# Kernel optimization log

Measured on AMD Instinct MI355X. Metric: run time of the kernel, lower is better.

The kernel has to match this reference:

```python
import jax, jax.numpy as jnp
import numpy as np

B, OBS, L, D, BINS, HID = 4096, 128, 4, 8, 16, 512
S = L * D  # max_seq_len = 32; qchunk_size = S, single Q chunk


def _lin(k, i, o, s):
    kw, kb = jax.random.split(k)
    return jax.random.normal(kw, (i, o), jnp.float32) * s, jnp.zeros((o,), jnp.float32)


def setup_inputs() -> dict:
    key = jax.random.key(0)
    ks = jax.random.split(key, 12)
    inp = {
        "obs": jax.random.normal(ks[0], (B, OBS), jnp.float32),
        "category": jax.random.randint(ks[1], (B, L, D), 0, BINS, jnp.int32),
    }
    # v_network: obs_dim -> 512 -> 512 -> 512 -> 1 (tanh hidden)
    dims_v = [OBS, HID, HID, HID, 1]
    for i in range(4):
        w, b = _lin(ks[2 + i], dims_v[i], dims_v[i + 1], 0.05)
        inp[f"v_w{i}"], inp[f"v_b{i}"] = w, b
    # q_network: (obs_dim+actor_dim) -> 512 -> 512 -> 512 -> bins*S
    dims_q = [OBS + D, HID, HID, HID, BINS * S]
    for i in range(4):
        w, b = _lin(ks[6 + i], dims_q[i], dims_q[i + 1], 0.05)
        inp[f"q_w{i}"], inp[f"q_b{i}"] = w, b
    return inp


def _mlp(x, ws, bs):
    for w, b in zip(ws[:-1], bs[:-1]):
        x = jnp.tanh(x @ w + b)
    return x @ ws[-1] + bs[-1]


def _actions_from_category(category):
    # zoom_in per (level, dim): width_l = 2/bins^(l+1); low accumulates cat*width.
    cat = category.astype(jnp.float32)  # (B, L, D)
    widths = 2.0 / (jnp.float32(BINS) ** jnp.arange(1, L + 1, dtype=jnp.float32))  # (L,)
    cum_low = jnp.cumsum(cat * widths[None, :, None], axis=1)  # (B, L, D)
    mids = -1.0 + cum_low + 0.5 * widths[None, :, None]  # midpoint after each level
    # mids_full[:, j, d] = midpoint of dim d after j zoom-in updates (j=0 -> 0.0)
    mids_full = jnp.concatenate(
        [jnp.zeros((category.shape[0], 1, D), jnp.float32), mids], axis=1)  # (B, L+1, D)
    # at sequence step k (input to Q), dim d' has had U[k,d'] updates
    k = jnp.arange(S)
    U = k[:, None] // D + (jnp.arange(D)[None, :] < (k[:, None] % D)).astype(jnp.int32)  # (S, D)
    dgrid = jnp.broadcast_to(jnp.arange(D)[None, :], (S, D))
    return mids_full[:, U, dgrid]  # (B, S, D)


def reference(obs, category,
              v_w0, v_b0, v_w1, v_b1, v_w2, v_b2, v_w3, v_b3,
              q_w0, q_b0, q_w1, q_b1, q_w2, q_b2, q_w3, q_b3):
    vw = [v_w0, v_w1, v_w2, v_w3]; vb = [v_b0, v_b1, v_b2, v_b3]
    qw = [q_w0, q_w1, q_w2, q_w3]; qb = [q_b0, q_b1, q_b2, q_b3]
    b = obs.shape[0]
    actions = _actions_from_category(category)  # (B, S, D)
    obs_rep = jnp.broadcast_to(obs[:, None, :], (b, S, OBS))
    x = jnp.concatenate([obs_rep, actions], axis=-1)  # (B, S, OBS+D)
    adv = _mlp(x, qw, qb)  # (B, S, S*BINS)
    adv = adv.reshape(b, S, S, BINS)
    s_idx = jnp.arange(S)
    adv = adv[:, s_idx, s_idx, :]  # diagonal gather -> (B, S, BINS)
    adv = adv.reshape(b, L, D, BINS)
    value = _mlp(obs, vw, vb)  # (B, 1)
    nbias = jnp.zeros((b, L, D, 1), jnp.float32)  # use_nbias=False
    return value, adv, nbias
```

## Files before the change

kernel.cpp:

```cpp
#include <hip/hip_runtime.h>
#include <hip/hip_bf16.h>

#define B_SZ   4096
#define OBS_N  128
#define HID    512
#define TANH_SCALE 2.885390081777927f


typedef __bf16 bf16x8_t __attribute__((ext_vector_type(8)));
typedef float  f32x4_t  __attribute__((ext_vector_type(4)));

__device__ inline float fast_tanh(float x) {
    float e = __builtin_amdgcn_exp2f(x * TANH_SCALE);
    return fmaf(-2.f, __builtin_amdgcn_rcpf(e + 1.f), 1.f);
}

__device__ inline float fast_tanh_pre(float x) {
    float e = __builtin_amdgcn_exp2f(x);
    return fmaf(-2.f, __builtin_amdgcn_rcpf(e + 1.f), 1.f);
}

__device__ inline void gld_lds16(const void* g, void* l) {
    __builtin_amdgcn_global_load_lds(
        (const __attribute__((address_space(1))) void*)g,
        (__attribute__((address_space(3))) void*)l, 16, 0, 0);
}

__device__ inline int hs_off(int row, int col) {
    int c = col >> 3;
    int phys = (c & ~7) | ((c ^ (row & 7)) & 7);
    return row * 512 + phys * 8 + (col & 7);
}

__global__ __launch_bounds__(256) void prep_kernel(
    const float* __restrict__ obs, const int* __restrict__ category,
    const float* __restrict__ qw0, const float* __restrict__ qb0,
    const float* __restrict__ qw1, const float* __restrict__ qw2,
    const float* __restrict__ qw3,
    const float* __restrict__ vw0, const float* __restrict__ vb0,
    const float* __restrict__ vw1, const float* __restrict__ vw2,
    const float* __restrict__ qb1, const float* __restrict__ qb2,
    const float* __restrict__ vb1, const float* __restrict__ vb2,
    __hip_bfloat16* __restrict__ obs_bf,
    __hip_bfloat16* __restrict__ w0t, __hip_bfloat16* __restrict__ w1t,
    __hip_bfloat16* __restrict__ w2t, __hip_bfloat16* __restrict__ w3t,
    __hip_bfloat16* __restrict__ vw0t, __hip_bfloat16* __restrict__ vw1t,
    __hip_bfloat16* __restrict__ vw2t,
    __hip_bfloat16* __restrict__ w0aug, __hip_bfloat16* __restrict__ vw0aug,
    __hip_bfloat16* __restrict__ acts_bf, float* __restrict__ bias_s,
    float* __restrict__ nbias)
{
    const int bid = blockIdx.x, tid = threadIdx.x;
    if (bid < 512) {
        int i = bid * 1024 + tid * 4;
        float4 v = *(const float4*)&obs[i];
        union { __hip_bfloat16 b[4]; uint2 u; } o;
        o.b[0] = __float2bfloat16(v.x);
        o.b[1] = __float2bfloat16(v.y);
        o.b[2] = __float2bfloat16(v.z);
        o.b[3] = __float2bfloat16(v.w);
        *(uint2*)&obs_bf[i] = o.u;
    } else if (bid < 1024) {
        const float* src = (bid < 768) ? qw0 : vw0;
        __hip_bfloat16* dst = (bid < 768) ? w0t : vw0t;
        int idx = ((bid - 512) & 255) * 256 + tid;
        int n = idx >> 7, k = idx & 127;
        dst[idx] = __float2bfloat16(src[k * 512 + n] * TANH_SCALE);
    } else if (bid < 6144) {
        int job = (bid - 1024) >> 10;
        const float* srcs[5] = {qw1, qw2, qw3, vw1, vw2};
        __hip_bfloat16* dsts[5] = {w1t, w2t, w3t, vw1t, vw2t};
        float sc = (job == 2) ? 1.0f : TANH_SCALE;
        int idx = ((bid - 1024) & 1023) * 256 + tid;
        int e    = idx & 7;
        int lane = (idx >> 3) & 63;
        int tile, kc;
        if (job == 2) {
            kc   = (idx >> 9) & 15;
            tile = idx >> 13;
        } else {
            int jj = (idx >> 9) & 3;
            kc     = (idx >> 11) & 15;
            int g  = idx >> 15;
            tile = g * 4 + jj;
        }
        int k = kc * 32 + (lane >> 4) * 8 + e;
        int n = tile * 16 + (lane & 15);
        dsts[job][idx] = __float2bfloat16(srcs[job][k * 512 + n] * sc);
    } else if (bid < 10240) {
        int t = (bid - 6144) * 256 + tid;
        int d = t & 7;
        int r = t >> 3;
        int b = r & 4095, s = r >> 12;
        int U = (s >> 3) + ((d < (s & 7)) ? 1 : 0);
        float a = 0.f;
        if (U > 0) {
            float w = 0.125f, cum = 0.f;
            for (int j = 0; j < U; ++j) {
                cum += (float)category[b * 32 + j * 8 + d] * w;
                if (j == U - 1) a = -1.f + cum + 0.5f * w;
                w *= 0.0625f;
            }
        }
        acts_bf[t] = __float2bfloat16(a);
    } else if (bid < 10368) {
        int sub = bid - 10240;
        bool isv = sub >= 64;
        int idx = (sub & 63) * 256 + tid;
        int e    = idx & 7;
        int lane = (idx >> 3) & 63;
        int tile = idx >> 9;
        int k = (lane >> 4) * 8 + e;
        int n = tile * 16 + (lane & 15);
        float v = 0.f;
        if (!isv) {
            if (k < 8) v = qw0[(128 + k) * 512 + n];
            else if (k == 8) v = qb0[n];
            w0aug[idx] = __float2bfloat16(v * TANH_SCALE);
        } else {
            if (k == 8) v = vb0[n];
            vw0aug[idx] = __float2bfloat16(v * TANH_SCALE);
        }
    } else if (bid < 10376) {
        int idx = (bid - 10368) * 256 + tid;
        const float* srcs[4] = {qb1, qb2, vb1, vb2};
        bias_s[idx] = srcs[idx >> 9][idx & 511] * TANH_SCALE;
    } else {
        int i = (bid - 10376) * 1024 + tid * 4;
        float4 z = {0.f, 0.f, 0.f, 0.f};
        *(float4*)&nbias[i] = z;
    }
}

__global__ __launch_bounds__(256) void gemm_dual(
    const __hip_bfloat16* __restrict__ A0, const __hip_bfloat16* __restrict__ B0,
    const float* __restrict__ bias0, void* __restrict__ C0, int K0, int epi0, int nb0,
    const __hip_bfloat16* __restrict__ A1, const __hip_bfloat16* __restrict__ B1,
    const float* __restrict__ bias1, void* __restrict__ C1, int K1, int epi1)
{
    __shared__ __hip_bfloat16 As[128 * 32];
    __shared__ __hip_bfloat16 Bs[128 * 32];

    const __hip_bfloat16 *A, *Bt;
    const float* bias;
    void* Cout;
    int K, epi, tb;
    if ((int)blockIdx.x < nb0) {
        A = A0; Bt = B0; bias = bias0; Cout = C0; K = K0; epi = epi0; tb = blockIdx.x;
    } else {
        A = A1; Bt = B1; bias = bias1; Cout = C1; K = K1; epi = epi1; tb = blockIdx.x - nb0;
    }
    const long m0 = (long)(tb >> 2) * 128;
    const int  n0 = (tb & 3) * 128;

    const int tid  = threadIdx.x;
    const int wave = tid >> 6, lane = tid & 63;
    const int quad = lane >> 4, t = lane & 15;
    const int wr = wave >> 1, wc = wave & 1;

    f32x4_t acc[4][4] = {};

    const int lrow  = lane >> 2;
    const int lkoff = (((lane & 3) + (lane >> 3)) & 3) * 8;

    const __hip_bfloat16* Ag0 = A  + (m0 + wave * 32 +      lrow) * (long)K + lkoff;
    const __hip_bfloat16* Ag1 = A  + (m0 + wave * 32 + 16 + lrow) * (long)K + lkoff;
    const __hip_bfloat16* Bg0 = Bt + (long)(n0 + wave * 32 +      lrow) * K + lkoff;
    const __hip_bfloat16* Bg1 = Bt + (long)(n0 + wave * 32 + 16 + lrow) * K + lkoff;
    __hip_bfloat16* AsB0 = &As[(wave * 32) * 32];
    __hip_bfloat16* AsB1 = &As[(wave * 32 + 16) * 32];
    __hip_bfloat16* BsB0 = &Bs[(wave * 32) * 32];
    __hip_bfloat16* BsB1 = &Bs[(wave * 32 + 16) * 32];

    const int slot = ((quad - (t >> 1)) & 3) * 8;

    for (int k0 = 0; k0 < K; k0 += 32) {
        gld_lds16(Ag0 + k0, AsB0);
        gld_lds16(Ag1 + k0, AsB1);
        gld_lds16(Bg0 + k0, BsB0);
        gld_lds16(Bg1 + k0, BsB1);
        __syncthreads();
        bf16x8_t af[4], bfr[4];
        #pragma unroll
        for (int i = 0; i < 4; ++i)
            af[i] = *(const bf16x8_t*)&As[(wr * 64 + i * 16 + t) * 32 + slot];
        #pragma unroll
        for (int j = 0; j < 4; ++j)
            bfr[j] = *(const bf16x8_t*)&Bs[(wc * 64 + j * 16 + t) * 32 + slot];
        #pragma unroll
        for (int i = 0; i < 4; ++i)
            #pragma unroll
            for (int j = 0; j < 4; ++j)
                acc[i][j] = __builtin_amdgcn_mfma_f32_16x16x32_bf16(af[i], bfr[j], acc[i][j], 0, 0, 0);
        __syncthreads();
    }

    #pragma unroll
    for (int i = 0; i < 4; ++i) {
        const long rbase = m0 + wr * 64 + i * 16 + quad * 4;
        #pragma unroll
        for (int j = 0; j < 4; ++j) {
            const int col = n0 + wc * 64 + j * 16 + t;
            #pragma unroll
            for (int r = 0; r < 4; ++r) {
                float v = acc[i][j][r];
                if (epi == 1) {
                    v = fast_tanh(v + bias[col]);
                    ((__hip_bfloat16*)Cout)[(rbase + r) * 512 + col] = __float2bfloat16(v);
                } else if (epi == 2) {
                    ((__hip_bfloat16*)Cout)[(rbase + r) * 512 + col] = __float2bfloat16(v);
                } else if (epi == 3) {
                    const long m = rbase + r;
                    const int brow = (int)(m & 63);
                    const long idx =
                        ((((m >> 6) * 8 + (col >> 6)) * 16 + (brow >> 4) * 4 + ((col >> 4) & 3)) * 256)
                        + ((col >> 2) & 3) * 64 + (brow & 15) * 4 + (col & 3);
                    ((float*)Cout)[idx] = v;
                } else {
                    ((float*)Cout)[(rbase + r) * 512 + col] = v;
                }
            }
        }
    }
}

__device__ inline void epi_store(
    __hip_bfloat16* hs, f32x4_t acc[4][4],
    int n0w, int quad, int t)
{
    #pragma unroll
    for (int j = 0; j < 4; ++j) {
        const int oc0 = n0w + j * 16 + quad * 4;
        const int cbase = oc0 >> 3;
        const int sub = (quad & 1) * 4;
        #pragma unroll
        for (int rt = 0; rt < 4; ++rt) {
            const int row = rt * 16 + t;
            union { __hip_bfloat16 b[4]; uint2 v; } o;
            o.b[0] = __float2bfloat16(fast_tanh_pre(acc[rt][j][0]));
            o.b[1] = __float2bfloat16(fast_tanh_pre(acc[rt][j][1]));
            o.b[2] = __float2bfloat16(fast_tanh_pre(acc[rt][j][2]));
            o.b[3] = __float2bfloat16(fast_tanh_pre(acc[rt][j][3]));
            const int phys = (cbase & ~7) | ((cbase ^ (row & 7)) & 7);
            *(uint2*)&hs[row * 512 + phys * 8 + sub] = o.v;
        }
    }
}

__device__ inline void mfma_layer(
    __hip_bfloat16* hs, const __hip_bfloat16* __restrict__ Wt,
    const float* __restrict__ bias_s, int w, int lane)
{
    const int quad = lane >> 4, t = lane & 15;
    const int n0w = w * 64;
    const __hip_bfloat16* Wl = Wt + (size_t)w * 32768 + (size_t)lane * 8;
    f32x4_t acc[4][4];
    #pragma unroll
    for (int j = 0; j < 4; ++j) {
        const f32x4_t bv = *(const f32x4_t*)&bias_s[n0w + j * 16 + quad * 4];
        #pragma unroll
        for (int rt = 0; rt < 4; ++rt)
            acc[rt][j] = bv;
    }
    bf16x8_t wA[4], wB[4];
    #pragma unroll
    for (int j = 0; j < 4; ++j) {
        wA[j] = *(const bf16x8_t*)(Wl + (size_t)(0 * 4 + j) * 512);
        wB[j] = *(const bf16x8_t*)(Wl + (size_t)(1 * 4 + j) * 512);
    }

    for (int m = 0; m < 8; ++m) {
        {
            const int kc = 2 * m;
            const int craw = kc * 4 + quad;
            const int phys = (craw & ~7) | ((craw ^ (t & 7)) & 7);
            const __hip_bfloat16* hrow = &hs[t * 512 + phys * 8];
            bf16x8_t a0 = *(const bf16x8_t*)(hrow);
            bf16x8_t a1 = *(const bf16x8_t*)(hrow + 8192);
            __builtin_amdgcn_s_setprio(1);
            #pragma unroll
            for (int j = 0; j < 4; ++j) {
                acc[0][j] = __builtin_amdgcn_mfma_f32_16x16x32_bf16(wA[j], a0, acc[0][j], 0, 0, 0);
                acc[1][j] = __builtin_amdgcn_mfma_f32_16x16x32_bf16(wA[j], a1, acc[1][j], 0, 0, 0);
            }
            bf16x8_t a2 = *(const bf16x8_t*)(hrow + 2 * 8192);
            bf16x8_t a3 = *(const bf16x8_t*)(hrow + 3 * 8192);
            #pragma unroll
            for (int j = 0; j < 4; ++j) {
                acc[2][j] = __builtin_amdgcn_mfma_f32_16x16x32_bf16(wA[j], a2, acc[2][j], 0, 0, 0);
                acc[3][j] = __builtin_amdgcn_mfma_f32_16x16x32_bf16(wA[j], a3, acc[3][j], 0, 0, 0);
            }
            __builtin_amdgcn_s_setprio(0);
            if (m < 7) {
                #pragma unroll
                for (int j = 0; j < 4; ++j)
                    wA[j] = *(const bf16x8_t*)(Wl + (size_t)((kc + 2) * 4 + j) * 512);
            }
        }
        {
            const int kc = 2 * m + 1;
            const int craw = kc * 4 + quad;
            const int phys = (craw & ~7) | ((craw ^ (t & 7)) & 7);
            const __hip_bfloat16* hrow = &hs[t * 512 + phys * 8];
            bf16x8_t a0 = *(const bf16x8_t*)(hrow);
            bf16x8_t a1 = *(const bf16x8_t*)(hrow + 8192);
            __builtin_amdgcn_s_setprio(1);
            #pragma unroll
            for (int j = 0; j < 4; ++j) {
                acc[0][j] = __builtin_amdgcn_mfma_f32_16x16x32_bf16(wB[j], a0, acc[0][j], 0, 0, 0);
                acc[1][j] = __builtin_amdgcn_mfma_f32_16x16x32_bf16(wB[j], a1, acc[1][j], 0, 0, 0);
            }
            bf16x8_t a2 = *(const bf16x8_t*)(hrow + 2 * 8192);
            bf16x8_t a3 = *(const bf16x8_t*)(hrow + 3 * 8192);
            #pragma unroll
            for (int j = 0; j < 4; ++j) {
                acc[2][j] = __builtin_amdgcn_mfma_f32_16x16x32_bf16(wB[j], a2, acc[2][j], 0, 0, 0);
                acc[3][j] = __builtin_amdgcn_mfma_f32_16x16x32_bf16(wB[j], a3, acc[3][j], 0, 0, 0);
            }
            __builtin_amdgcn_s_setprio(0);
            if (m < 7) {
                #pragma unroll
                for (int j = 0; j < 4; ++j)
                    wB[j] = *(const bf16x8_t*)(Wl + (size_t)((kc + 2) * 4 + j) * 512);
            }
        }
    }
    __syncthreads();
    epi_store(hs, acc, n0w, quad, t);
    __syncthreads();
}

__global__ __launch_bounds__(512, 4) void fused_kernel(
    const float* __restrict__ p,
    const float* __restrict__ pv,
    const __hip_bfloat16* __restrict__ acts_bf,
    const __hip_bfloat16* __restrict__ w0aug,
    const __hip_bfloat16* __restrict__ vw0aug,
    const __hip_bfloat16* __restrict__ w1t, const float* __restrict__ qb1s,
    const __hip_bfloat16* __restrict__ w2t, const float* __restrict__ qb2s,
    const __hip_bfloat16* __restrict__ w3t, const float* __restrict__ qb3,
    float* __restrict__ advout,
    const __hip_bfloat16* __restrict__ vw1t, const float* __restrict__ vb1s,
    const __hip_bfloat16* __restrict__ vw2t, const float* __restrict__ vb2s,
    const float* __restrict__ vw3, const float* __restrict__ vb3,
    float* __restrict__ vout)
{
    __shared__ __hip_bfloat16 hs[64 * 512];
    const int bid = blockIdx.x;
    const int tid = threadIdx.x;
    const int w = tid >> 6, lane = tid & 63;
    const int quad = lane >> 4, t = lane & 15;
    const bool is_q = bid < 2048;
    const int s  = is_q ? (bid >> 6) : 0;
    const int mb = is_q ? (bid & 63) : (bid - 2048);
    const int n0w = w * 64;

    {
        const float* Pt = (is_q ? p : pv) + (((size_t)mb * 8 + w) * 16) * 256 + lane * 4;
        const __hip_bfloat16* W0 = is_q ? w0aug : vw0aug;
        f32x4_t acc[4][4];
        #pragma unroll
        for (int rt = 0; rt < 4; ++rt)
            #pragma unroll
            for (int j = 0; j < 4; ++j)
                acc[rt][j] = *(const f32x4_t*)(Pt + (rt * 4 + j) * 256);
        bf16x8_t bfrag[4];
        #pragma unroll
        for (int rt = 0; rt < 4; ++rt) {
            union { bf16x8_t vec; unsigned short u[8]; } bu;
            #pragma unroll
            for (int i = 0; i < 8; ++i) bu.u[i] = 0;
            if (quad == 1) bu.u[0] = 0x3F80;
            if (is_q && quad == 0) {
                const long r = (long)s * 4096 + mb * 64 + rt * 16 + t;
                bu.vec = *(const bf16x8_t*)&acts_bf[r * 8];
            }
            bfrag[rt] = bu.vec;
        }
        bf16x8_t wq[4];
        #pragma unroll
        for (int j = 0; j < 4; ++j)
            wq[j] = *(const bf16x8_t*)(W0 + ((size_t)(w * 4 + j) * 64 + lane) * 8);
        __builtin_amdgcn_s_setprio(1);
        #pragma unroll
        for (int j = 0; j < 4; ++j)
            #pragma unroll
            for (int rt = 0; rt < 4; ++rt)
                acc[rt][j] = __builtin_amdgcn_mfma_f32_16x16x32_bf16(wq[j], bfrag[rt], acc[rt][j], 0, 0, 0);
        __builtin_amdgcn_s_setprio(0);
        epi_store(hs, acc, n0w, quad, t);
    }
    __syncthreads();

    mfma_layer(hs, is_q ? w1t : vw1t, is_q ? qb1s : vb1s, w, lane);
    mfma_layer(hs, is_q ? w2t : vw2t, is_q ? qb2s : vb2s, w, lane);

    if (is_q) {
        f32x4_t acc = {};
        {
            const __hip_bfloat16* W3l = w3t + ((size_t)s * 16 * 64 + (size_t)lane) * 8;
            const int kc0 = (w >> 2) * 8;
            const int wrow = (w & 3) * 16 + t;
            #pragma unroll
            for (int kk = 0; kk < 8; ++kk) {
                const int kc = kc0 + kk;
                const int craw = kc * 4 + quad;
                const int phys = (craw & ~7) | ((craw ^ (t & 7)) & 7);
                bf16x8_t a = *(const bf16x8_t*)&hs[wrow * 512 + phys * 8];
                bf16x8_t bq = *(const bf16x8_t*)(W3l + (size_t)kc * 512);
                acc = __builtin_amdgcn_mfma_f32_16x16x32_bf16(a, bq, acc, 0, 0, 0);
            }
        }
        __syncthreads();
        float* hsf = (float*)hs;
        {
            const float add = (w < 4) ? qb3[s * 16 + t] : 0.f;
            const int base = (w >> 2) * 1024;
            #pragma unroll
            for (int rr = 0; rr < 4; ++rr)
                hsf[base + ((w & 3) * 16 + quad * 4 + rr) * 16 + t] = acc[rr] + add;
        }
        __syncthreads();
        const int row = tid >> 3, cp = tid & 7;
        float2 lo = *(const float2*)&hsf[row * 16 + cp * 2];
        float2 hi = *(const float2*)&hsf[1024 + row * 16 + cp * 2];
        float2 v2 = {lo.x + hi.x, lo.y + hi.y};
        *(float2*)&advout[(size_t)(mb * 64 + row) * 512 + s * 16 + cp * 2] = v2;
    } else {
        const int row = tid >> 3, seg = tid & 7;
        float sum = 0.f;
        for (int k = seg * 64; k < seg * 64 + 64; ++k)
            sum += __bfloat162float(hs[hs_off(row, k)]) * vw3[k];
        sum += __shfl_xor(sum, 1);
        sum += __shfl_xor(sum, 2);
        sum += __shfl_xor(sum, 4);
        if (seg == 0) vout[mb * 64 + row] = sum + vb3[0];
    }
}

extern "C" void kernel_launch(void* const* d_in, const int* in_sizes, int n_in,
                              void* d_out, int out_size, void* d_ws, size_t ws_size,
                              hipStream_t stream) {
    const float* obs      = (const float*)d_in[0];
    const int*   category = (const int*)d_in[1];
    const float* v_w0 = (const float*)d_in[2];
    const float* v_b0 = (const float*)d_in[3];
    const float* v_w1 = (const float*)d_in[4];
    const float* v_b1 = (const float*)d_in[5];
    const float* v_w2 = (const float*)d_in[6];
    const float* v_b2 = (const float*)d_in[7];
    const float* v_w3 = (const float*)d_in[8];
    const float* v_b3 = (const float*)d_in[9];
    const float* q_w0 = (const float*)d_in[10];
    const float* q_b0 = (const float*)d_in[11];
    const float* q_w1 = (const float*)d_in[12];
    const float* q_b1 = (const float*)d_in[13];
    const float* q_w2 = (const float*)d_in[14];
    const float* q_b2 = (const float*)d_in[15];
    const float* q_w3 = (const float*)d_in[16];
    const float* q_b3 = (const float*)d_in[17];

    char* ws = (char*)d_ws;
    __hip_bfloat16* obs_bf = (__hip_bfloat16*)(ws + 0);
    __hip_bfloat16* w0t    = (__hip_bfloat16*)(ws + 1048576);
    __hip_bfloat16* vw0t   = (__hip_bfloat16*)(ws + 1179648);
    __hip_bfloat16* w1t    = (__hip_bfloat16*)(ws + 1310720);
    __hip_bfloat16* w2t    = (__hip_bfloat16*)(ws + 1835008);
    __hip_bfloat16* w3t    = (__hip_bfloat16*)(ws + 2359296);
    __hip_bfloat16* vw1t   = (__hip_bfloat16*)(ws + 2883584);
    __hip_bfloat16* vw2t   = (__hip_bfloat16*)(ws + 3407872);
    __hip_bfloat16* w0aug  = (__hip_bfloat16*)(ws + 3932160);
    __hip_bfloat16* vw0aug = (__hip_bfloat16*)(ws + 3964928);
    __hip_bfloat16* acts_bf= (__hip_bfloat16*)(ws + 3997696);
    float*          p      = (float*)         (ws + 6094848);
    float*          pv     = (float*)         (ws + 14483456);
    float*          bias_s = (float*)         (ws + 22872064);

    float* out       = (float*)d_out;
    float* out_value = out;
    float* out_adv   = out + 4096;
    float* out_nbias = out + 4096 + (size_t)B_SZ * 512;

    prep_kernel<<<10504, 256, 0, stream>>>(
        obs, category, q_w0, q_b0, q_w1, q_w2, q_w3, v_w0, v_b0, v_w1, v_w2,
        q_b1, q_b2, v_b1, v_b2,
        obs_bf, w0t, w1t, w2t, w3t, vw0t, vw1t, vw2t, w0aug, vw0aug,
        acts_bf, bias_s, out_nbias);

    gemm_dual<<<256, 256, 0, stream>>>(
        obs_bf, w0t, nullptr, p, 128, 3, 128,
        obs_bf, vw0t, nullptr, pv, 128, 3);

    fused_kernel<<<2112, 512, 0, stream>>>(
        p, pv, acts_bf, w0aug, vw0aug,
        w1t, bias_s, w2t, bias_s + 512, w3t, q_b3, out_adv,
        vw1t, bias_s + 1024, vw2t, bias_s + 1536, v_w3, v_b3, out_value);
}
```

Measured before the change: 253.5 us.

## Fold first-layer obs GEMM into fused kernel, dropping separate gemm_dual pass

Removes the standalone gemm_dual launch that precomputed obs@W0 into fp32 workspace buffers, which the fused kernel then reloaded per sequence step. Instead each fused block computes the obs projection directly with MFMA over K=128, plus the action/bias augmentation chunk, using a new K-chunked pre-tiled W0 layout built in prep. This saves a kernel launch and about 16MB of fp32 intermediate write+read. In exchange it recomputes the obs projection for every sequence step (32x redundant MFMA work for the Q path).

```diff
diff --git a/kernel.cpp b/kernel.cpp
--- a/kernel.cpp
+++ b/kernel.cpp
@@ -10,20 +10,9 @@
 typedef __bf16 bf16x8_t __attribute__((ext_vector_type(8)));
 typedef float  f32x4_t  __attribute__((ext_vector_type(4)));
 
-__device__ inline float fast_tanh(float x) {
-    float e = __builtin_amdgcn_exp2f(x * TANH_SCALE);
-    return fmaf(-2.f, __builtin_amdgcn_rcpf(e + 1.f), 1.f);
-}
-
 __device__ inline float fast_tanh_pre(float x) {
     float e = __builtin_amdgcn_exp2f(x);
     return fmaf(-2.f, __builtin_amdgcn_rcpf(e + 1.f), 1.f);
-}
-
-__device__ inline void gld_lds16(const void* g, void* l) {
-    __builtin_amdgcn_global_load_lds(
-        (const __attribute__((address_space(1))) void*)g,
-        (__attribute__((address_space(3))) void*)l, 16, 0, 0);
 }
 
 __device__ inline int hs_off(int row, int col) {
@@ -42,11 +31,10 @@
     const float* __restrict__ qb1, const float* __restrict__ qb2,
     const float* __restrict__ vb1, const float* __restrict__ vb2,
     __hip_bfloat16* __restrict__ obs_bf,
-    __hip_bfloat16* __restrict__ w0t, __hip_bfloat16* __restrict__ w1t,
-    __hip_bfloat16* __restrict__ w2t, __hip_bfloat16* __restrict__ w3t,
-    __hip_bfloat16* __restrict__ vw0t, __hip_bfloat16* __restrict__ vw1t,
-    __hip_bfloat16* __restrict__ vw2t,
-    __hip_bfloat16* __restrict__ w0aug, __hip_bfloat16* __restrict__ vw0aug,
+    __hip_bfloat16* __restrict__ w1t, __hip_bfloat16* __restrict__ w2t,
+    __hip_bfloat16* __restrict__ w3t,
+    __hip_bfloat16* __restrict__ vw1t, __hip_bfloat16* __restrict__ vw2t,
+    __hip_bfloat16* __restrict__ w0ta, __hip_bfloat16* __restrict__ vw0ta,
     __hip_bfloat16* __restrict__ acts_bf, float* __restrict__ bias_s,
     float* __restrict__ nbias)
 {
@@ -60,18 +48,12 @@
         o.b[2] = __float2bfloat16(v.z);
         o.b[3] = __float2bfloat16(v.w);
         *(uint2*)&obs_bf[i] = o.u;
-    } else if (bid < 1024) {
-        const float* src = (bid < 768) ? qw0 : vw0;
-        __hip_bfloat16* dst = (bid < 768) ? w0t : vw0t;
-        int idx = ((bid - 512) & 255) * 256 + tid;
-        int n = idx >> 7, k = idx & 127;
-        dst[idx] = __float2bfloat16(src[k * 512 + n] * TANH_SCALE);
-    } else if (bid < 6144) {
-        int job = (bid - 1024) >> 10;
+    } else if (bid < 5632) {
+        int job = (bid - 512) >> 10;
         const float* srcs[5] = {qw1, qw2, qw3, vw1, vw2};
         __hip_bfloat16* dsts[5] = {w1t, w2t, w3t, vw1t, vw2t};
         float sc = (job == 2) ? 1.0f : TANH_SCALE;
-        int idx = ((bid - 1024) & 1023) * 256 + tid;
+        int idx = ((bid - 512) & 1023) * 256 + tid;
         int e    = idx & 7;
         int lane = (idx >> 3) & 63;
         int tile, kc;
@@ -87,8 +69,8 @@
         int k = kc * 32 + (lane >> 4) * 8 + e;
         int n = tile * 16 + (lane & 15);
         dsts[job][idx] = __float2bfloat16(srcs[job][k * 512 + n] * sc);
-    } else if (bid < 10240) {
-        int t = (bid - 6144) * 256 + tid;
+    } else if (bid < 9728) {
+        int t = (bid - 5632) * 256 + tid;
         int d = t & 7;
         int r = t >> 3;
         int b = r & 4095, s = r >> 12;
@@ -104,22 +86,24 @@
         }
         acts_bf[t] = __float2bfloat16(a);
     } else if (bid < 10368) {
-        int sub = bid - 10240;
-        bool isv = sub >= 64;
-        int idx = (sub & 63) * 256 + tid;
+        int sub = bid - 9728;
+        bool isv = sub >= 320;
+        int idx = (isv ? sub - 320 : sub) * 256 + tid;
         int e    = idx & 7;
         int lane = (idx >> 3) & 63;
-        int tile = idx >> 9;
-        int k = (lane >> 4) * 8 + e;
-        int n = tile * 16 + (lane & 15);
+        int j    = (idx >> 9) & 3;
+        int kcw  = idx >> 11;
+        int k = (kcw % 5) * 32 + (lane >> 4) * 8 + e;
+        int n = ((kcw / 5) * 4 + j) * 16 + (lane & 15);
         float v = 0.f;
         if (!isv) {
-            if (k < 8) v = qw0[(128 + k) * 512 + n];
-            else if (k == 8) v = qb0[n];
-            w0aug[idx] = __float2bfloat16(v * TANH_SCALE);
+            if (k < 136) v = qw0[k * 512 + n];
+            else if (k == 136) v = qb0[n];
+            w0ta[idx] = __float2bfloat16(v * TANH_SCALE);
         } else {
-            if (k == 8) v = vb0[n];
-            vw0aug[idx] = __float2bfloat16(v * TANH_SCALE);
+            if (k < 128) v = vw0[k * 512 + n];
+            else if (k == 136) v = vb0[n];
+            vw0ta[idx] = __float2bfloat16(v * TANH_SCALE);
         }
     } else if (bid < 10376) {
         int idx = (bid - 10368) * 256 + tid;
@@ -129,98 +113,6 @@
         int i = (bid - 10376) * 1024 + tid * 4;
         float4 z = {0.f, 0.f, 0.f, 0.f};
         *(float4*)&nbias[i] = z;
-    }
-}
-
-__global__ __launch_bounds__(256) void gemm_dual(
-    const __hip_bfloat16* __restrict__ A0, const __hip_bfloat16* __restrict__ B0,
-    const float* __restrict__ bias0, void* __restrict__ C0, int K0, int epi0, int nb0,
-    const __hip_bfloat16* __restrict__ A1, const __hip_bfloat16* __restrict__ B1,
-    const float* __restrict__ bias1, void* __restrict__ C1, int K1, int epi1)
-{
-    __shared__ __hip_bfloat16 As[128 * 32];
-    __shared__ __hip_bfloat16 Bs[128 * 32];
-
-    const __hip_bfloat16 *A, *Bt;
-    const float* bias;
-    void* Cout;
-    int K, epi, tb;
-    if ((int)blockIdx.x < nb0) {
-        A = A0; Bt = B0; bias = bias0; Cout = C0; K = K0; epi = epi0; tb = blockIdx.x;
-    } else {
-        A = A1; Bt = B1; bias = bias1; Cout = C1; K = K1; epi = epi1; tb = blockIdx.x - nb0;
-    }
-    const long m0 = (long)(tb >> 2) * 128;
-    const int  n0 = (tb & 3) * 128;
-
-    const int tid  = threadIdx.x;
-    const int wave = tid >> 6, lane = tid & 63;
-    const int quad = lane >> 4, t = lane & 15;
-    const int wr = wave >> 1, wc = wave & 1;
-
-    f32x4_t acc[4][4] = {};
-
-    const int lrow  = lane >> 2;
-    const int lkoff = (((lane & 3) + (lane >> 3)) & 3) * 8;
-
-    const __hip_bfloat16* Ag0 = A  + (m0 + wave * 32 +      lrow) * (long)K + lkoff;
-    const __hip_bfloat16* Ag1 = A  + (m0 + wave * 32 + 16 + lrow) * (long)K + lkoff;
-    const __hip_bfloat16* Bg0 = Bt + (long)(n0 + wave * 32 +      lrow) * K + lkoff;
-    const __hip_bfloat16* Bg1 = Bt + (long)(n0 + wave * 32 + 16 + lrow) * K + lkoff;
-    __hip_bfloat16* AsB0 = &As[(wave * 32) * 32];
-    __hip_bfloat16* AsB1 = &As[(wave * 32 + 16) * 32];
-    __hip_bfloat16* BsB0 = &Bs[(wave * 32) * 32];
-    __hip_bfloat16* BsB1 = &Bs[(wave * 32 + 16) * 32];
-
-    const int slot = ((quad - (t >> 1)) & 3) * 8;
-
-    for (int k0 = 0; k0 < K; k0 += 32) {
-        gld_lds16(Ag0 + k0, AsB0);
-        gld_lds16(Ag1 + k0, AsB1);
-        gld_lds16(Bg0 + k0, BsB0);
-        gld_lds16(Bg1 + k0, BsB1);
-        __syncthreads();
-        bf16x8_t af[4], bfr[4];
-        #pragma unroll
-        for (int i = 0; i < 4; ++i)
-            af[i] = *(const bf16x8_t*)&As[(wr * 64 + i * 16 + t) * 32 + slot];
-        #pragma unroll
-        for (int j = 0; j < 4; ++j)
-            bfr[j] = *(const bf16x8_t*)&Bs[(wc * 64 + j * 16 + t) * 32 + slot];
-        #pragma unroll
-        for (int i = 0; i < 4; ++i)
-            #pragma unroll
-            for (int j = 0; j < 4; ++j)
-                acc[i][j] = __builtin_amdgcn_mfma_f32_16x16x32_bf16(af[i], bfr[j], acc[i][j], 0, 0, 0);
-        __syncthreads();
-    }
-
-    #pragma unroll
-    for (int i = 0; i < 4; ++i) {
-        const long rbase = m0 + wr * 64 + i * 16 + quad * 4;
-        #pragma unroll
-        for (int j = 0; j < 4; ++j) {
-            const int col = n0 + wc * 64 + j * 16 + t;
-            #pragma unroll
-            for (int r = 0; r < 4; ++r) {
-                float v = acc[i][j][r];
-                if (epi == 1) {
-                    v = fast_tanh(v + bias[col]);
-                    ((__hip_bfloat16*)Cout)[(rbase + r) * 512 + col] = __float2bfloat16(v);
-                } else if (epi == 2) {
-                    ((__hip_bfloat16*)Cout)[(rbase + r) * 512 + col] = __float2bfloat16(v);
-                } else if (epi == 3) {
-                    const long m = rbase + r;
-                    const int brow = (int)(m & 63);
-                    const long idx =
-                        ((((m >> 6) * 8 + (col >> 6)) * 16 + (brow >> 4) * 4 + ((col >> 4) & 3)) * 256)
-                        + ((col >> 2) & 3) * 64 + (brow & 15) * 4 + (col & 3);
-                    ((float*)Cout)[idx] = v;
-                } else {
-                    ((float*)Cout)[(rbase + r) * 512 + col] = v;
-                }
-            }
-        }
     }
 }
 
@@ -331,11 +223,10 @@
 }
 
 __global__ __launch_bounds__(512, 4) void fused_kernel(
-    const float* __restrict__ p,
-    const float* __restrict__ pv,
+    const __hip_bfloat16* __restrict__ obs_bf,
     const __hip_bfloat16* __restrict__ acts_bf,
-    const __hip_bfloat16* __restrict__ w0aug,
-    const __hip_bfloat16* __restrict__ vw0aug,
+    const __hip_bfloat16* __restrict__ w0ta,
+    const __hip_bfloat16* __restrict__ vw0ta,
     const __hip_bfloat16* __restrict__ w1t, const float* __restrict__ qb1s,
     const __hip_bfloat16* __restrict__ w2t, const float* __restrict__ qb2s,
     const __hip_bfloat16* __restrict__ w3t, const float* __restrict__ qb3,
@@ -356,38 +247,81 @@
     const int n0w = w * 64;
 
     {
-        const float* Pt = (is_q ? p : pv) + (((size_t)mb * 8 + w) * 16) * 256 + lane * 4;
-        const __hip_bfloat16* W0 = is_q ? w0aug : vw0aug;
-        f32x4_t acc[4][4];
+        const __hip_bfloat16* W0 = is_q ? w0ta : vw0ta;
+        const __hip_bfloat16* Wl = W0 + (size_t)w * 10240 + (size_t)lane * 8;
+        const __hip_bfloat16* ob = obs_bf + ((size_t)(mb * 64) + t) * 128 + quad * 8;
+        f32x4_t acc[4][4] = {};
+        bf16x8_t wA[4], wB[4];
         #pragma unroll
-        for (int rt = 0; rt < 4; ++rt)
+        for (int j = 0; j < 4; ++j) {
+            wA[j] = *(const bf16x8_t*)(Wl + (size_t)(0 * 4 + j) * 512);
+            wB[j] = *(const bf16x8_t*)(Wl + (size_t)(1 * 4 + j) * 512);
+        }
+        #pragma unroll
+        for (int m = 0; m < 2; ++m) {
+            {
+                const int kc = 2 * m;
+                bf16x8_t a0 = *(const bf16x8_t*)(ob + 0 * 16 * 128 + kc * 32);
+                bf16x8_t a1 = *(const bf16x8_t*)(ob + 1 * 16 * 128 + kc * 32);
+                bf16x8_t a2 = *(const bf16x8_t*)(ob + 2 * 16 * 128 + kc * 32);
+                bf16x8_t a3 = *(const bf16x8_t*)(ob + 3 * 16 * 128 + kc * 32);
+                __builtin_amdgcn_s_setprio(1);
+                #pragma unroll
+                for (int j = 0; j < 4; ++j) {
+                    acc[0][j] = __builtin_amdgcn_mfma_f32_16x16x32_bf16(wA[j], a0, acc[0][j], 0, 0, 0);
+                    acc[1][j] = __builtin_amdgcn_mfma_f32_16x16x32_bf16(wA[j], a1, acc[1][j], 0, 0, 0);
+                    acc[2][j] = __builtin_amdgcn_mfma_f32_16x16x32_bf16(wA[j], a2, acc[2][j], 0, 0, 0);
+                    acc[3][j] = __builtin_amdgcn_mfma_f32_16x16x32_bf16(wA[j], a3, acc[3][j], 0, 0, 0);
+                }
+                __builtin_amdgcn_s_setprio(0);
+                #pragma unroll
+                for (int j = 0; j < 4; ++j)
+                    wA[j] = *(const bf16x8_t*)(Wl + (size_t)((kc + 2) * 4 + j) * 512);
+            }
+            {
+                const int kc = 2 * m + 1;
+                bf16x8_t a0 = *(const bf16x8_t*)(ob + 0 * 16 * 128 + kc * 32);
+                bf16x8_t a1 = *(const bf16x8_t*)(ob + 1 * 16 * 128 + kc * 32);
+                bf16x8_t a2 = *(const bf16x8_t*)(ob + 2 * 16 * 128 + kc * 32);
+                bf16x8_t a3 = *(const bf16x8_t*)(ob + 3 * 16 * 128 + kc * 32);
+                __builtin_amdgcn_s_setprio(1);
+                #pragma unroll
+                for (int j = 0; j < 4; ++j) {
+                    acc[0][j] = __builtin_amdgcn_mfma_f32_16x16x32_bf16(wB[j], a0, acc[0][j], 0, 0, 0);
+                    acc[1][j] = __builtin_amdgcn_mfma_f32_16x16x32_bf16(wB[j], a1, acc[1][j], 0, 0, 0);
+                    acc[2][j] = __builtin_amdgcn_mfma_f32_16x16x32_bf16(wB[j], a2, acc[2][j], 0, 0, 0);
+                    acc[3][j] = __builtin_amdgcn_mfma_f32_16x16x32_bf16(wB[j], a3, acc[3][j], 0, 0, 0);
+                }
+                __builtin_amdgcn_s_setprio(0);
+                if (m == 0) {
+                    #pragma unroll
+                    for (int j = 0; j < 4; ++j)
+                        wB[j] = *(const bf16x8_t*)(Wl + (size_t)(3 * 4 + j) * 512);
+                }
+            }
+        }
+        {
+            bf16x8_t bfrag[4];
+            #pragma unroll
+            for (int rt = 0; rt < 4; ++rt) {
+                union { bf16x8_t vec; unsigned short u[8]; } bu;
+                #pragma unroll
+                for (int i = 0; i < 8; ++i) bu.u[i] = 0;
+                if (quad == 1) bu.u[0] = 0x3F80;
+                if (is_q && quad == 0) {
+                    const long r = (long)s * 4096 + mb * 64 + rt * 16 + t;
+                    bu.vec = *(const bf16x8_t*)&acts_bf[r * 8];
+                }
+                bfrag[rt] = bu.vec;
+            }
+            __builtin_amdgcn_s_setprio(1);
             #pragma unroll
             for (int j = 0; j < 4; ++j)
-                acc[rt][j] = *(const f32x4_t*)(Pt + (rt * 4 + j) * 256);
-        bf16x8_t bfrag[4];
-        #pragma unroll
-        for (int rt = 0; rt < 4; ++rt) {
-            union { bf16x8_t vec; unsigned short u[8]; } bu;
-            #pragma unroll
-            for (int i = 0; i < 8; ++i) bu.u[i] = 0;
-            if (quad == 1) bu.u[0] = 0x3F80;
-            if (is_q && quad == 0) {
-                const long r = (long)s * 4096 + mb * 64 + rt * 16 + t;
-                bu.vec = *(const bf16x8_t*)&acts_bf[r * 8];
-            }
-            bfrag[rt] = bu.vec;
-        }
-        bf16x8_t wq[4];
-        #pragma unroll
-        for (int j = 0; j < 4; ++j)
-            wq[j] = *(const bf16x8_t*)(W0 + ((size_t)(w * 4 + j) * 64 + lane) * 8);
-        __builtin_amdgcn_s_setprio(1);
-        #pragma unroll
-        for (int j = 0; j < 4; ++j)
-            #pragma unroll
-            for (int rt = 0; rt < 4; ++rt)
-                acc[rt][j] = __builtin_amdgcn_mfma_f32_16x16x32_bf16(wq[j], bfrag[rt], acc[rt][j], 0, 0, 0);
-        __builtin_amdgcn_s_setprio(0);
+                #pragma unroll
+                for (int rt = 0; rt < 4; ++rt)
+                    acc[rt][j] = __builtin_amdgcn_mfma_f32_16x16x32_bf16(wA[j], bfrag[rt], acc[rt][j], 0, 0, 0);
+            __builtin_amdgcn_s_setprio(0);
+        }
         epi_store(hs, acc, n0w, quad, t);
     }
     __syncthreads();
@@ -462,19 +396,15 @@
 
     char* ws = (char*)d_ws;
     __hip_bfloat16* obs_bf = (__hip_bfloat16*)(ws + 0);
-    __hip_bfloat16* w0t    = (__hip_bfloat16*)(ws + 1048576);
-    __hip_bfloat16* vw0t   = (__hip_bfloat16*)(ws + 1179648);
-    __hip_bfloat16* w1t    = (__hip_bfloat16*)(ws + 1310720);
-    __hip_bfloat16* w2t    = (__hip_bfloat16*)(ws + 1835008);
-    __hip_bfloat16* w3t    = (__hip_bfloat16*)(ws + 2359296);
-    __hip_bfloat16* vw1t   = (__hip_bfloat16*)(ws + 2883584);
-    __hip_bfloat16* vw2t   = (__hip_bfloat16*)(ws + 3407872);
-    __hip_bfloat16* w0aug  = (__hip_bfloat16*)(ws + 3932160);
-    __hip_bfloat16* vw0aug = (__hip_bfloat16*)(ws + 3964928);
+    __hip_bfloat16* w1t    = (__hip_bfloat16*)(ws + 1048576);
+    __hip_bfloat16* w2t    = (__hip_bfloat16*)(ws + 1572864);
+    __hip_bfloat16* w3t    = (__hip_bfloat16*)(ws + 2097152);
+    __hip_bfloat16* vw1t   = (__hip_bfloat16*)(ws + 2621440);
+    __hip_bfloat16* vw2t   = (__hip_bfloat16*)(ws + 3145728);
+    __hip_bfloat16* w0ta   = (__hip_bfloat16*)(ws + 3670016);
+    __hip_bfloat16* vw0ta  = (__hip_bfloat16*)(ws + 3833856);
     __hip_bfloat16* acts_bf= (__hip_bfloat16*)(ws + 3997696);
-    float*          p      = (float*)         (ws + 6094848);
-    float*          pv     = (float*)         (ws + 14483456);
-    float*          bias_s = (float*)         (ws + 22872064);
+    float*          bias_s = (float*)         (ws + 6094848);
 
     float* out       = (float*)d_out;
     float* out_value = out;
@@ -484,15 +414,11 @@
     prep_kernel<<<10504, 256, 0, stream>>>(
         obs, category, q_w0, q_b0, q_w1, q_w2, q_w3, v_w0, v_b0, v_w1, v_w2,
         q_b1, q_b2, v_b1, v_b2,
-        obs_bf, w0t, w1t, w2t, w3t, vw0t, vw1t, vw2t, w0aug, vw0aug,
+        obs_bf, w1t, w2t, w3t, vw1t, vw2t, w0ta, vw0ta,
         acts_bf, bias_s, out_nbias);
 
-    gemm_dual<<<256, 256, 0, stream>>>(
-        obs_bf, w0t, nullptr, p, 128, 3, 128,
-        obs_bf, vw0t, nullptr, pv, 128, 3);
-
     fused_kernel<<<2112, 512, 0, stream>>>(
-        p, pv, acts_bf, w0aug, vw0aug,
+        obs_bf, acts_bf, w0ta, vw0ta,
         w1t, bias_s, w2t, bias_s + 512, w3t, q_b3, out_adv,
         vw1t, bias_s + 1024, vw2t, bias_s + 1536, v_w3, v_b3, out_value);
 }
```

After: 259.4 us. 2.3% more time.

## Fold first-layer obs GEMM into prep kernel with on-the-fly bf16 conversion

Applied to the files above, without the earlier changes.

Removes the separate gemm_dual launch and the obs/w0 bf16 staging buffers. The first 256 blocks of prep_kernel now compute the obs x W0 products directly, converting fp32 obs and scaled, transposed W0 to bf16 while filling LDS. This saves one kernel launch and a round trip through global memory for the converted operands. In exchange the loads are strided scalar fp32 reads with no async LDS copy, and the GEMM blocks share a launch with the prep blocks.

```diff
diff --git a/kernel.cpp b/kernel.cpp
--- a/kernel.cpp
+++ b/kernel.cpp
@@ -10,20 +10,9 @@
 typedef __bf16 bf16x8_t __attribute__((ext_vector_type(8)));
 typedef float  f32x4_t  __attribute__((ext_vector_type(4)));
 
-__device__ inline float fast_tanh(float x) {
-    float e = __builtin_amdgcn_exp2f(x * TANH_SCALE);
-    return fmaf(-2.f, __builtin_amdgcn_rcpf(e + 1.f), 1.f);
-}
-
 __device__ inline float fast_tanh_pre(float x) {
     float e = __builtin_amdgcn_exp2f(x);
     return fmaf(-2.f, __builtin_amdgcn_rcpf(e + 1.f), 1.f);
-}
-
-__device__ inline void gld_lds16(const void* g, void* l) {
-    __builtin_amdgcn_global_load_lds(
-        (const __attribute__((address_space(1))) void*)g,
-        (__attribute__((address_space(3))) void*)l, 16, 0, 0);
 }
 
 __device__ inline int hs_off(int row, int col) {
@@ -41,37 +30,112 @@
     const float* __restrict__ vw1, const float* __restrict__ vw2,
     const float* __restrict__ qb1, const float* __restrict__ qb2,
     const float* __restrict__ vb1, const float* __restrict__ vb2,
-    __hip_bfloat16* __restrict__ obs_bf,
-    __hip_bfloat16* __restrict__ w0t, __hip_bfloat16* __restrict__ w1t,
-    __hip_bfloat16* __restrict__ w2t, __hip_bfloat16* __restrict__ w3t,
-    __hip_bfloat16* __restrict__ vw0t, __hip_bfloat16* __restrict__ vw1t,
-    __hip_bfloat16* __restrict__ vw2t,
+    __hip_bfloat16* __restrict__ w1t, __hip_bfloat16* __restrict__ w2t,
+    __hip_bfloat16* __restrict__ w3t,
+    __hip_bfloat16* __restrict__ vw1t, __hip_bfloat16* __restrict__ vw2t,
     __hip_bfloat16* __restrict__ w0aug, __hip_bfloat16* __restrict__ vw0aug,
     __hip_bfloat16* __restrict__ acts_bf, float* __restrict__ bias_s,
-    float* __restrict__ nbias)
+    float* __restrict__ nbias,
+    float* __restrict__ p, float* __restrict__ pv)
 {
+    __shared__ __hip_bfloat16 Asg[128 * 32];
+    __shared__ __hip_bfloat16 Bsg[128 * 32];
     const int bid = blockIdx.x, tid = threadIdx.x;
-    if (bid < 512) {
-        int i = bid * 1024 + tid * 4;
-        float4 v = *(const float4*)&obs[i];
-        union { __hip_bfloat16 b[4]; uint2 u; } o;
-        o.b[0] = __float2bfloat16(v.x);
-        o.b[1] = __float2bfloat16(v.y);
-        o.b[2] = __float2bfloat16(v.z);
-        o.b[3] = __float2bfloat16(v.w);
-        *(uint2*)&obs_bf[i] = o.u;
-    } else if (bid < 1024) {
-        const float* src = (bid < 768) ? qw0 : vw0;
-        __hip_bfloat16* dst = (bid < 768) ? w0t : vw0t;
-        int idx = ((bid - 512) & 255) * 256 + tid;
-        int n = idx >> 7, k = idx & 127;
-        dst[idx] = __float2bfloat16(src[k * 512 + n] * TANH_SCALE);
-    } else if (bid < 6144) {
-        int job = (bid - 1024) >> 10;
+    if (bid < 256) {
+        const bool isq = bid < 128;
+        const int tb = bid & 127;
+        const long m0 = (long)(tb >> 2) * 128;
+        const int  n0 = (tb & 3) * 128;
+        const float* Wsrc = isq ? qw0 : vw0;
+        float* Cout = isq ? p : pv;
+
+        const int wave = tid >> 6, lane = tid & 63;
+        const int quad = lane >> 4, t = lane & 15;
+        const int wr = wave >> 1, wc = wave & 1;
+        const int slot = ((quad - (t >> 1)) & 3) * 8;
+
+        f32x4_t acc[4][4] = {};
+        const int r = tid >> 1;
+        const int h = tid & 1;
+
+        for (int k0 = 0; k0 < 128; k0 += 32) {
+            #pragma unroll
+            for (int cc = 0; cc < 2; ++cc) {
+                const int c = 2 * h + cc;
+                const float* src = &obs[(m0 + r) * 128 + k0 + c * 8];
+                float4 v0 = *(const float4*)(src);
+                float4 v1 = *(const float4*)(src + 4);
+                union { __hip_bfloat16 b[8]; uint4 u; } ob;
+                ob.b[0] = __float2bfloat16(v0.x); ob.b[1] = __float2bfloat16(v0.y);
+                ob.b[2] = __float2bfloat16(v0.z); ob.b[3] = __float2bfloat16(v0.w);
+                ob.b[4] = __float2bfloat16(v1.x); ob.b[5] = __float2bfloat16(v1.y);
+                ob.b[6] = __float2bfloat16(v1.z); ob.b[7] = __float2bfloat16(v1.w);
+                *(uint4*)&Asg[r * 32 + ((c - (r >> 1)) & 3) * 8] = ob.u;
+            }
+            #pragma unroll
+            for (int cc = 0; cc < 2; ++cc) {
+                const int c = 2 * h + cc;
+                union { __hip_bfloat16 b[8]; uint4 u; } wb;
+                #pragma unroll
+                for (int e = 0; e < 8; ++e)
+                    wb.b[e] = __float2bfloat16(
+                        Wsrc[(size_t)(k0 + c * 8 + e) * 512 + n0 + r] * TANH_SCALE);
+                *(uint4*)&Bsg[r * 32 + ((c - (r >> 1)) & 3) * 8] = wb.u;
+            }
+            __syncthreads();
+            bf16x8_t af[4], bfr[4];
+            #pragma unroll
+            for (int i = 0; i < 4; ++i)
+                af[i] = *(const bf16x8_t*)&Asg[(wr * 64 + i * 16 + t) * 32 + slot];
+            #pragma unroll
+            for (int j = 0; j < 4; ++j)
+                bfr[j] = *(const bf16x8_t*)&Bsg[(wc * 64 + j * 16 + t) * 32 + slot];
+            #pragma unroll
+            for (int i = 0; i < 4; ++i)
+                #pragma unroll
+                for (int j = 0; j < 4; ++j)
+                    acc[i][j] = __builtin_amdgcn_mfma_f32_16x16x32_bf16(af[i], bfr[j], acc[i][j], 0, 0, 0);
+            __syncthreads();
+        }
+        #pragma unroll
+        for (int i = 0; i < 4; ++i) {
+            const long rbase = m0 + wr * 64 + i * 16 + quad * 4;
+            #pragma unroll
+            for (int j = 0; j < 4; ++j) {
+                const int col = n0 + wc * 64 + j * 16 + t;
+                #pragma unroll
+                for (int rr = 0; rr < 4; ++rr) {
+                    const long m = rbase + rr;
+                    const int brow = (int)(m & 63);
+                    const long idx =
+                        ((((m >> 6) * 8 + (col >> 6)) * 16 + (brow >> 4) * 4 + ((col >> 4) & 3)) * 256)
+                        + ((col >> 2) & 3) * 64 + (brow & 15) * 4 + (col & 3);
+                    Cout[idx] = acc[i][j][rr];
+                }
+            }
+        }
+    } else if (bid < 4352) {
+        int t = (bid - 256) * 256 + tid;
+        int d = t & 7;
+        int r = t >> 3;
+        int b = r & 4095, s = r >> 12;
+        int U = (s >> 3) + ((d < (s & 7)) ? 1 : 0);
+        float a = 0.f;
+        if (U > 0) {
+            float w = 0.125f, cum = 0.f;
+            for (int j = 0; j < U; ++j) {
+                cum += (float)category[b * 32 + j * 8 + d] * w;
+                if (j == U - 1) a = -1.f + cum + 0.5f * w;
+                w *= 0.0625f;
+            }
+        }
+        acts_bf[t] = __float2bfloat16(a);
+    } else if (bid < 9472) {
+        int job = (bid - 4352) >> 10;
         const float* srcs[5] = {qw1, qw2, qw3, vw1, vw2};
         __hip_bfloat16* dsts[5] = {w1t, w2t, w3t, vw1t, vw2t};
         float sc = (job == 2) ? 1.0f : TANH_SCALE;
-        int idx = ((bid - 1024) & 1023) * 256 + tid;
+        int idx = ((bid - 4352) & 1023) * 256 + tid;
         int e    = idx & 7;
         int lane = (idx >> 3) & 63;
         int tile, kc;
@@ -87,24 +151,8 @@
         int k = kc * 32 + (lane >> 4) * 8 + e;
         int n = tile * 16 + (lane & 15);
         dsts[job][idx] = __float2bfloat16(srcs[job][k * 512 + n] * sc);
-    } else if (bid < 10240) {
-        int t = (bid - 6144) * 256 + tid;
-        int d = t & 7;
-        int r = t >> 3;
-        int b = r & 4095, s = r >> 12;
-        int U = (s >> 3) + ((d < (s & 7)) ? 1 : 0);
-        float a = 0.f;
-        if (U > 0) {
-            float w = 0.125f, cum = 0.f;
-            for (int j = 0; j < U; ++j) {
-                cum += (float)category[b * 32 + j * 8 + d] * w;
-                if (j == U - 1) a = -1.f + cum + 0.5f * w;
-                w *= 0.0625f;
-            }
-        }
-        acts_bf[t] = __float2bfloat16(a);
-    } else if (bid < 10368) {
-        int sub = bid - 10240;
+    } else if (bid < 9600) {
+        int sub = bid - 9472;
         bool isv = sub >= 64;
         int idx = (sub & 63) * 256 + tid;
         int e    = idx & 7;
@@ -121,106 +169,14 @@
             if (k == 8) v = vb0[n];
             vw0aug[idx] = __float2bfloat16(v * TANH_SCALE);
         }
-    } else if (bid < 10376) {
-        int idx = (bid - 10368) * 256 + tid;
+    } else if (bid < 9608) {
+        int idx = (bid - 9600) * 256 + tid;
         const float* srcs[4] = {qb1, qb2, vb1, vb2};
         bias_s[idx] = srcs[idx >> 9][idx & 511] * TANH_SCALE;
     } else {
-        int i = (bid - 10376) * 1024 + tid * 4;
+        int i = (bid - 9608) * 1024 + tid * 4;
         float4 z = {0.f, 0.f, 0.f, 0.f};
         *(float4*)&nbias[i] = z;
-    }
-}
-
-__global__ __launch_bounds__(256) void gemm_dual(
-    const __hip_bfloat16* __restrict__ A0, const __hip_bfloat16* __restrict__ B0,
-    const float* __restrict__ bias0, void* __restrict__ C0, int K0, int epi0, int nb0,
-    const __hip_bfloat16* __restrict__ A1, const __hip_bfloat16* __restrict__ B1,
-    const float* __restrict__ bias1, void* __restrict__ C1, int K1, int epi1)
-{
-    __shared__ __hip_bfloat16 As[128 * 32];
-    __shared__ __hip_bfloat16 Bs[128 * 32];
-
-    const __hip_bfloat16 *A, *Bt;
-    const float* bias;
-    void* Cout;
-    int K, epi, tb;
-    if ((int)blockIdx.x < nb0) {
-        A = A0; Bt = B0; bias = bias0; Cout = C0; K = K0; epi = epi0; tb = blockIdx.x;
-    } else {
-        A = A1; Bt = B1; bias = bias1; Cout = C1; K = K1; epi = epi1; tb = blockIdx.x - nb0;
-    }
-    const long m0 = (long)(tb >> 2) * 128;
-    const int  n0 = (tb & 3) * 128;
-
-    const int tid  = threadIdx.x;
-    const int wave = tid >> 6, lane = tid & 63;
-    const int quad = lane >> 4, t = lane & 15;
-    const int wr = wave >> 1, wc = wave & 1;
-
-    f32x4_t acc[4][4] = {};
-
-    const int lrow  = lane >> 2;
-    const int lkoff = (((lane & 3) + (lane >> 3)) & 3) * 8;
-
-    const __hip_bfloat16* Ag0 = A  + (m0 + wave * 32 +      lrow) * (long)K + lkoff;
-    const __hip_bfloat16* Ag1 = A  + (m0 + wave * 32 + 16 + lrow) * (long)K + lkoff;
-    const __hip_bfloat16* Bg0 = Bt + (long)(n0 + wave * 32 +      lrow) * K + lkoff;
-    const __hip_bfloat16* Bg1 = Bt + (long)(n0 + wave * 32 + 16 + lrow) * K + lkoff;
-    __hip_bfloat16* AsB0 = &As[(wave * 32) * 32];
-    __hip_bfloat16* AsB1 = &As[(wave * 32 + 16) * 32];
-    __hip_bfloat16* BsB0 = &Bs[(wave * 32) * 32];
-    __hip_bfloat16* BsB1 = &Bs[(wave * 32 + 16) * 32];
-
-    const int slot = ((quad - (t >> 1)) & 3) * 8;
-
-    for (int k0 = 0; k0 < K; k0 += 32) {
-        gld_lds16(Ag0 + k0, AsB0);
-        gld_lds16(Ag1 + k0, AsB1);
-        gld_lds16(Bg0 + k0, BsB0);
-        gld_lds16(Bg1 + k0, BsB1);
-        __syncthreads();
-        bf16x8_t af[4], bfr[4];
-        #pragma unroll
-        for (int i = 0; i < 4; ++i)
-            af[i] = *(const bf16x8_t*)&As[(wr * 64 + i * 16 + t) * 32 + slot];
-        #pragma unroll
-        for (int j = 0; j < 4; ++j)
-            bfr[j] = *(const bf16x8_t*)&Bs[(wc * 64 + j * 16 + t) * 32 + slot];
-        #pragma unroll
-        for (int i = 0; i < 4; ++i)
-            #pragma unroll
-            for (int j = 0; j < 4; ++j)
-                acc[i][j] = __builtin_amdgcn_mfma_f32_16x16x32_bf16(af[i], bfr[j], acc[i][j], 0, 0, 0);
-        __syncthreads();
-    }
-
-    #pragma unroll
-    for (int i = 0; i < 4; ++i) {
-        const long rbase = m0 + wr * 64 + i * 16 + quad * 4;
-        #pragma unroll
-        for (int j = 0; j < 4; ++j) {
-            const int col = n0 + wc * 64 + j * 16 + t;
-            #pragma unroll
-            for (int r = 0; r < 4; ++r) {
-                float v = acc[i][j][r];
-                if (epi == 1) {
-                    v = fast_tanh(v + bias[col]);
-                    ((__hip_bfloat16*)Cout)[(rbase + r) * 512 + col] = __float2bfloat16(v);
-                } else if (epi == 2) {
-                    ((__hip_bfloat16*)Cout)[(rbase + r) * 512 + col] = __float2bfloat16(v);
-                } else if (epi == 3) {
-                    const long m = rbase + r;
-                    const int brow = (int)(m & 63);
-                    const long idx =
-                        ((((m >> 6) * 8 + (col >> 6)) * 16 + (brow >> 4) * 4 + ((col >> 4) & 3)) * 256)
-                        + ((col >> 2) & 3) * 64 + (brow & 15) * 4 + (col & 3);
-                    ((float*)Cout)[idx] = v;
-                } else {
-                    ((float*)Cout)[(rbase + r) * 512 + col] = v;
-                }
-            }
-        }
     }
 }
 
@@ -461,35 +417,28 @@
     const float* q_b3 = (const float*)d_in[17];
 
     char* ws = (char*)d_ws;
-    __hip_bfloat16* obs_bf = (__hip_bfloat16*)(ws + 0);
-    __hip_bfloat16* w0t    = (__hip_bfloat16*)(ws + 1048576);
-    __hip_bfloat16* vw0t   = (__hip_bfloat16*)(ws + 1179648);
-    __hip_bfloat16* w1t    = (__hip_bfloat16*)(ws + 1310720);
-    __hip_bfloat16* w2t    = (__hip_bfloat16*)(ws + 1835008);
-    __hip_bfloat16* w3t    = (__hip_bfloat16*)(ws + 2359296);
-    __hip_bfloat16* vw1t   = (__hip_bfloat16*)(ws + 2883584);
-    __hip_bfloat16* vw2t   = (__hip_bfloat16*)(ws + 3407872);
-    __hip_bfloat16* w0aug  = (__hip_bfloat16*)(ws + 3932160);
-    __hip_bfloat16* vw0aug = (__hip_bfloat16*)(ws + 3964928);
-    __hip_bfloat16* acts_bf= (__hip_bfloat16*)(ws + 3997696);
-    float*          p      = (float*)         (ws + 6094848);
-    float*          pv     = (float*)         (ws + 14483456);
-    float*          bias_s = (float*)         (ws + 22872064);
+    __hip_bfloat16* w1t    = (__hip_bfloat16*)(ws + 0);
+    __hip_bfloat16* w2t    = (__hip_bfloat16*)(ws + 524288);
+    __hip_bfloat16* w3t    = (__hip_bfloat16*)(ws + 1048576);
+    __hip_bfloat16* vw1t   = (__hip_bfloat16*)(ws + 1572864);
+    __hip_bfloat16* vw2t   = (__hip_bfloat16*)(ws + 2097152);
+    __hip_bfloat16* w0aug  = (__hip_bfloat16*)(ws + 2621440);
+    __hip_bfloat16* vw0aug = (__hip_bfloat16*)(ws + 2654208);
+    __hip_bfloat16* acts_bf= (__hip_bfloat16*)(ws + 2686976);
+    float*          bias_s = (float*)         (ws + 4784128);
+    float*          p      = (float*)         (ws + 4792320);
+    float*          pv     = (float*)         (ws + 13180928);
 
     float* out       = (float*)d_out;
     float* out_value = out;
     float* out_adv   = out + 4096;
     float* out_nbias = out + 4096 + (size_t)B_SZ * 512;
 
-    prep_kernel<<<10504, 256, 0, stream>>>(
+    prep_kernel<<<9736, 256, 0, stream>>>(
         obs, category, q_w0, q_b0, q_w1, q_w2, q_w3, v_w0, v_b0, v_w1, v_w2,
         q_b1, q_b2, v_b1, v_b2,
-        obs_bf, w0t, w1t, w2t, w3t, vw0t, vw1t, vw2t, w0aug, vw0aug,
-        acts_bf, bias_s, out_nbias);
-
-    gemm_dual<<<256, 256, 0, stream>>>(
-        obs_bf, w0t, nullptr, p, 128, 3, 128,
-        obs_bf, vw0t, nullptr, pv, 128, 3);
+        w1t, w2t, w3t, vw1t, vw2t, w0aug, vw0aug,
+        acts_bf, bias_s, out_nbias, p, pv);
 
     fused_kernel<<<2112, 512, 0, stream>>>(
         p, pv, acts_bf, w0aug, vw0aug,
```

After: 252.5 us. Within noise of the previous version (-0.4%).
